# Kernel tuning notes

Hardware: AMD Instinct MI355X
Metric: run time of the kernel (lower is better)

## Reference

```python
import jax, jax.numpy as jnp
import numpy as np

N_NODES = 50000

def setup_inputs() -> dict:
    key = jax.random.key(0)
    ks = jax.random.split(key, 9)
    x = jax.random.normal(ks[0], (N_NODES, 100), dtype=jnp.float32)
    W0 = jax.random.normal(ks[1], (100, 64), dtype=jnp.float32) * (1.0 / np.sqrt(100))
    b0 = jnp.zeros((64,), dtype=jnp.float32)
    W1 = jax.random.normal(ks[2], (64, 64), dtype=jnp.float32) * (1.0 / np.sqrt(64))
    b1 = jnp.zeros((64,), dtype=jnp.float32)
    W2 = jax.random.normal(ks[3], (64, 47), dtype=jnp.float32) * (1.0 / np.sqrt(64))
    b2 = jnp.zeros((47,), dtype=jnp.float32)
    src = jax.random.randint(ks[4], (800000,), 0, N_NODES, dtype=jnp.int64)
    dst = jax.random.randint(ks[5], (800000,), 0, N_NODES, dtype=jnp.int64)
    return {"x": x, "W0": W0, "b0": b0, "W1": W1, "b1": b1,
            "W2": W2, "b2": b2, "src": src, "dst": dst}

def _degree_norms(src, dst, n_nodes):
    ones = jnp.ones(src.shape[0], dtype=jnp.float32)
    deg_out = jax.ops.segment_sum(ones, src, num_segments=n_nodes)
    deg_in = jax.ops.segment_sum(ones, dst, num_segments=n_nodes)
    # DGL GraphConv norm='both': clamp degree to >= 1 then D^{-1/2}
    norm_src = jax.lax.rsqrt(jnp.maximum(deg_out, 1.0))  # [N]
    norm_dst = jax.lax.rsqrt(jnp.maximum(deg_in, 1.0))   # [N]
    return norm_src, norm_dst

def _graph_conv(h, W, b, src, dst, norm_src, norm_dst, n_nodes):
    # h: [N, F_in] -> D_in^{-1/2} A D_out^{-1/2} h W + b
    m = h * norm_src[:, None]                              # [N, F_in]
    agg = jax.ops.segment_sum(m[src], dst, num_segments=n_nodes)  # SpMM gather/scatter
    agg = agg * norm_dst[:, None]
    return agg @ W + b

def reference(x, W0, b0, W1, b1, W2, b2, src, dst):
    n = x.shape[0]
    norm_src, norm_dst = _degree_norms(src, dst, n)
    # dropout is identity in eval mode (deterministic reference)
    h = jax.nn.relu(_graph_conv(x, W0, b0, src, dst, norm_src, norm_dst, n))
    h = jax.nn.relu(_graph_conv(h, W1, b1, src, dst, norm_src, norm_dst, n))
    out = _graph_conv(h, W2, b2, src, dst, norm_src, norm_dst, n)
    return out
```

## Files before the change

### kernel.cpp

```cpp
#include <hip/hip_runtime.h>
#include <hip/hip_fp16.h>
#include <stdint.h>


#define NNODES 50000
#define NBW    12500
#define HT     1024
#define EPT    7
#define EPB    (HT * EPT)

struct __align__(8) h4pack { __half2 a, b; };

__global__ __launch_bounds__(HT) void hist_kernel(
        const int* __restrict__ src, const int* __restrict__ dst,
        unsigned* __restrict__ cnt_dst, unsigned* __restrict__ cnt_src,
        unsigned char* __restrict__ rank, int E) {
    __shared__ unsigned h[NBW];
    const int b = blockIdx.x, base = b * EPB;
    int s[EPT], d[EPT]; bool val[EPT]; unsigned char rk[EPT];
    #pragma unroll
    for (int j = 0; j < EPT; ++j) {
        int e = base + j * HT + (int)threadIdx.x;
        val[j] = (e < E);
        s[j] = val[j] ? src[e] : 0;
        d[j] = val[j] ? dst[e] : 0;
        rk[j] = 0;
    }
    for (int w = threadIdx.x; w < NBW; w += HT) h[w] = 0u;
    __syncthreads();
    #pragma unroll
    for (int j = 0; j < EPT; ++j) if (val[j]) {
        unsigned sh = 8u * (d[j] & 3);
        unsigned old = atomicAdd(&h[d[j] >> 2], 1u << sh);
        rk[j] = (unsigned char)((old >> sh) & 0xffu);
    }
    __syncthreads();
    for (int w = threadIdx.x; w < NBW; w += HT) {
        cnt_dst[(size_t)b * NBW + w] = h[w];
        h[w] = 0u;
    }
    __syncthreads();
    #pragma unroll
    for (int j = 0; j < EPT; ++j) if (val[j])
        atomicAdd(&h[s[j] >> 2], 1u << (8u * (s[j] & 3)));
    #pragma unroll
    for (int j = 0; j < EPT; ++j) {
        int e = base + j * HT + (int)threadIdx.x;
        if (val[j]) rank[e] = rk[j];
    }
    __syncthreads();
    for (int w = threadIdx.x; w < NBW; w += HT)
        cnt_src[(size_t)b * NBW + w] = h[w];
}

__global__ __launch_bounds__(1024) void merge_scan_kernel(
        unsigned* __restrict__ cnt_dst, const unsigned* __restrict__ cnt_src,
        int* __restrict__ row_off, int* __restrict__ blocksum,
        float* __restrict__ ns, float* __restrict__ nd, int hb) {
    const int t = threadIdx.x;
    const int half = t & 511;
    const int w = blockIdx.x * 512 + half;
    const bool is_dst = (t < 512);
    unsigned deg[4] = {0, 0, 0, 0};
    if (w < NBW) {
        if (is_dst) {
            for (int b = 0; b < hb; ++b) {
                unsigned v = cnt_dst[(size_t)b * NBW + w];
                cnt_dst[(size_t)b * NBW + w] =
                    deg[0] | (deg[1] << 8) | (deg[2] << 16) | (deg[3] << 24);
                #pragma unroll
                for (int k = 0; k < 4; ++k) deg[k] += (v >> (8 * k)) & 0xffu;
            }
            #pragma unroll
            for (int k = 0; k < 4; ++k)
                nd[4 * w + k] = rsqrtf((float)(deg[k] < 1u ? 1u : deg[k]));
        } else {
            for (int b = 0; b < hb; ++b) {
                unsigned v = cnt_src[(size_t)b * NBW + w];
                #pragma unroll
                for (int k = 0; k < 4; ++k) deg[k] += (v >> (8 * k)) & 0xffu;
            }
            #pragma unroll
            for (int k = 0; k < 4; ++k)
                ns[4 * w + k] = rsqrtf((float)(deg[k] < 1u ? 1u : deg[k]));
        }
    }
    __shared__ int wsum[8];
    int sum = (is_dst && w < NBW) ? (int)(deg[0] + deg[1] + deg[2] + deg[3]) : 0;
    int lane = t & 63, wv = t >> 6;
    int incl = sum;
    #pragma unroll
    for (int off = 1; off < 64; off <<= 1) {
        int x = __shfl_up(incl, off, 64);
        if (lane >= off) incl += x;
    }
    if (is_dst && lane == 63) wsum[wv] = incl;
    __syncthreads();
    if (t < 8) {
        int v = wsum[t], ic = v;
        #pragma unroll
        for (int off = 1; off < 8; off <<= 1) {
            int x = __shfl_up(ic, off, 8);
            if ((t & 7) >= off) ic += x;
        }
        wsum[t] = ic;
    }
    __syncthreads();
    if (is_dst && w < NBW) {
        int base = (wv > 0 ? wsum[wv - 1] : 0) + incl - sum;
        row_off[4 * w + 0] = base;
        row_off[4 * w + 1] = base + (int)deg[0];
        row_off[4 * w + 2] = base + (int)(deg[0] + deg[1]);
        row_off[4 * w + 3] = base + (int)(deg[0] + deg[1] + deg[2]);
    }
    if (t == 0) blocksum[blockIdx.x] = wsum[7];
}

__global__ void scan2_kernel(const int* __restrict__ blocksum,
                             int* __restrict__ blockoff, int nb) {
    int i = threadIdx.x;
    int v = (i < nb) ? blocksum[i] : 0;
    int incl = v;
    #pragma unroll
    for (int off = 1; off < 64; off <<= 1) {
        int x = __shfl_up(incl, off, 64);
        if (i >= off) incl += x;
    }
    if (i < nb) blockoff[i] = incl - v;
}

__global__ __launch_bounds__(HT) void scatter_kernel(
        const int* __restrict__ src, const int* __restrict__ dst,
        const unsigned* __restrict__ cnt_dst, const int* __restrict__ row_off,
        const int* __restrict__ blockoff, const unsigned char* __restrict__ rank,
        unsigned short* __restrict__ src_sorted, int E) {
    const int b = blockIdx.x, base = b * EPB;
    #pragma unroll
    for (int j = 0; j < EPT; ++j) {
        int e = base + j * HT + (int)threadIdx.x;
        if (e >= E) continue;
        int d = dst[e];
        unsigned pk = cnt_dst[(size_t)b * NBW + (d >> 2)];
        unsigned pfx = (pk >> (8u * (d & 3))) & 0xffu;
        unsigned p = (unsigned)(row_off[d] + blockoff[d >> 11]) + pfx + (unsigned)rank[e];
        src_sorted[p] = (unsigned short)src[e];
    }
}

__global__ __launch_bounds__(256) void row_sort_kernel(
        const int* __restrict__ row_off, const int* __restrict__ blockoff,
        unsigned short* __restrict__ srcs, int n, int E) {
    int node = (blockIdx.x * 256 + threadIdx.x) >> 6;
    int lane = threadIdx.x & 63;
    if (node >= n) return;
    int beg = row_off[node] + blockoff[node >> 11];
    int end = (node + 1 < n) ? row_off[node + 1] + blockoff[(node + 1) >> 11] : E;
    int len = end - beg;
    if (len <= 1) return;
    unsigned v = (lane < len) ? (unsigned)srcs[beg + lane] : 0xffffffffu;
    #pragma unroll
    for (int k = 2; k <= 64; k <<= 1) {
        #pragma unroll
        for (int j = k >> 1; j >= 1; j >>= 1) {
            unsigned o = __shfl_xor(v, j, 64);
            bool down  = (lane & k) != 0;
            bool lower = (lane & j) == 0;
            unsigned mn = (v < o) ? v : o;
            unsigned mx = (v < o) ? o : v;
            v = (lower != down) ? mn : mx;
        }
    }
    if (lane < len) srcs[beg + lane] = (unsigned short)v;
}

template <int FIN, int FOUT>
__global__ __launch_bounds__(256) void rowscale_gemm_h(const float* __restrict__ H,
        const float* __restrict__ ns, const float* __restrict__ Wg,
        __half* __restrict__ T, int n) {
    constexpr int WS = (FOUT + 3) & ~3;
    constexpr int RP = FIN + 4;
    constexpr int Q  = FIN / 4;
    __shared__ __align__(16) float Wlds[FIN * WS];
    __shared__ __align__(16) float rows[64 * RP];

    for (int i = threadIdx.x; i < FIN * WS; i += 256) {
        int k = i / WS, j = i - k * WS;
        Wlds[i] = (j < FOUT) ? Wg[k * FOUT + j] : 0.0f;
    }
    int node0 = blockIdx.x * 64;
    for (int idx = threadIdx.x; idx < 64 * Q; idx += 256) {
        int nl = idx / Q, q = idx - nl * Q;
        int node = node0 + nl;
        float4 v = make_float4(0.f, 0.f, 0.f, 0.f);
        float s = 0.f;
        if (node < n) {
            v = *(const float4*)&H[(size_t)node * FIN + 4 * q];
            s = ns[node];
        }
        float4* d4 = (float4*)&rows[nl * RP + 4 * q];
        d4->x = v.x * s; d4->y = v.y * s; d4->z = v.z * s; d4->w = v.w * s;
    }
    __syncthreads();

    int w = threadIdx.x >> 6;
    int lane = threadIdx.x & 63;
    int g = lane >> 4, f = lane & 15;
    if (4 * f < WS) {
        float4 acc0 = make_float4(0.f,0.f,0.f,0.f), acc1 = acc0, acc2 = acc0, acc3 = acc0;
        const float* r0 = &rows[(w * 16 + 0 * 4 + g) * RP];
        const float* r1 = &rows[(w * 16 + 1 * 4 + g) * RP];
        const float* r2 = &rows[(w * 16 + 2 * 4 + g) * RP];
        const float* r3 = &rows[(w * 16 + 3 * 4 + g) * RP];
        for (int k = 0; k < FIN; ++k) {
            float4 wv = *(const float4*)&Wlds[k * WS + 4 * f];
            float h0 = r0[k], h1 = r1[k], h2 = r2[k], h3 = r3[k];
            acc0.x += h0 * wv.x; acc0.y += h0 * wv.y; acc0.z += h0 * wv.z; acc0.w += h0 * wv.w;
            acc1.x += h1 * wv.x; acc1.y += h1 * wv.y; acc1.z += h1 * wv.z; acc1.w += h1 * wv.w;
            acc2.x += h2 * wv.x; acc2.y += h2 * wv.y; acc2.z += h2 * wv.z; acc2.w += h2 * wv.w;
            acc3.x += h3 * wv.x; acc3.y += h3 * wv.y; acc3.z += h3 * wv.z; acc3.w += h3 * wv.w;
        }
        float4 accs[4] = {acc0, acc1, acc2, acc3};
        #pragma unroll
        for (int r = 0; r < 4; ++r) {
            int node = node0 + w * 16 + r * 4 + g;
            if (node < n) {
                h4pack pk;
                pk.a = __float22half2_rn(make_float2(accs[r].x, accs[r].y));
                pk.b = __float22half2_rn(make_float2(accs[r].z, accs[r].w));
                *(h4pack*)&T[(size_t)node * WS + 4 * f] = pk;
            }
        }
    }
}

__global__ __launch_bounds__(256) void agg_mid_kernel(const __half* __restrict__ T,
        const int* __restrict__ row_off, const int* __restrict__ blockoff,
        const unsigned short* __restrict__ srcs, const float* __restrict__ nd,
        const float* __restrict__ bias, float* __restrict__ H, int n, int E) {
    int node = (blockIdx.x * 256 + threadIdx.x) >> 6;
    int lane = threadIdx.x & 63;
    int g = lane >> 4, f = lane & 15;
    if (node >= n) return;
    int beg = row_off[node] + blockoff[node >> 11];
    int end = (node + 1 < n) ? row_off[node + 1] + blockoff[(node + 1) >> 11] : E;
    float4 acc = make_float4(0.f, 0.f, 0.f, 0.f);
    float4 acc2 = acc;
    int e = beg + g;
    for (; e + 4 < end; e += 8) {
        int s0 = srcs[e], s1 = srcs[e + 4];
        h4pack r0 = *(const h4pack*)&T[(size_t)s0 * 64 + 4 * f];
        h4pack r1 = *(const h4pack*)&T[(size_t)s1 * 64 + 4 * f];
        float2 a0 = __half22float2(r0.a), a1 = __half22float2(r0.b);
        float2 b0 = __half22float2(r1.a), b1 = __half22float2(r1.b);
        acc.x  += a0.x; acc.y  += a0.y; acc.z  += a1.x; acc.w  += a1.y;
        acc2.x += b0.x; acc2.y += b0.y; acc2.z += b1.x; acc2.w += b1.y;
    }
    if (e < end) {
        h4pack r0 = *(const h4pack*)&T[(size_t)srcs[e] * 64 + 4 * f];
        float2 a0 = __half22float2(r0.a), a1 = __half22float2(r0.b);
        acc.x += a0.x; acc.y += a0.y; acc.z += a1.x; acc.w += a1.y;
    }
    acc.x += acc2.x; acc.y += acc2.y; acc.z += acc2.z; acc.w += acc2.w;
    #pragma unroll
    for (int m = 16; m <= 32; m <<= 1) {
        acc.x += __shfl_xor(acc.x, m, 64);
        acc.y += __shfl_xor(acc.y, m, 64);
        acc.z += __shfl_xor(acc.z, m, 64);
        acc.w += __shfl_xor(acc.w, m, 64);
    }
    if (g == 0) {
        float sd = nd[node];
        float4 o;
        o.x = fmaxf(fmaf(acc.x, sd, bias[4 * f + 0]), 0.f);
        o.y = fmaxf(fmaf(acc.y, sd, bias[4 * f + 1]), 0.f);
        o.z = fmaxf(fmaf(acc.z, sd, bias[4 * f + 2]), 0.f);
        o.w = fmaxf(fmaf(acc.w, sd, bias[4 * f + 3]), 0.f);
        *(float4*)&H[(size_t)node * 64 + 4 * f] = o;
    }
}

__global__ __launch_bounds__(256) void agg_final_kernel(const __half* __restrict__ T,
        const int* __restrict__ row_off, const int* __restrict__ blockoff,
        const unsigned short* __restrict__ srcs, const float* __restrict__ nd,
        const float* __restrict__ bias, float* __restrict__ Out, int n, int E) {
    int node = (blockIdx.x * 256 + threadIdx.x) >> 6;
    int lane = threadIdx.x & 63;
    int g = lane >> 4, f = lane & 15;
    if (node >= n) return;
    int beg = row_off[node] + blockoff[node >> 11];
    int end = (node + 1 < n) ? row_off[node + 1] + blockoff[(node + 1) >> 11] : E;
    float4 acc = make_float4(0.f, 0.f, 0.f, 0.f);
    float4 acc2 = acc;
    if (f < 12) {
        int e = beg + g;
        for (; e + 4 < end; e += 8) {
            int s0 = srcs[e], s1 = srcs[e + 4];
            h4pack r0 = *(const h4pack*)&T[(size_t)s0 * 48 + 4 * f];
            h4pack r1 = *(const h4pack*)&T[(size_t)s1 * 48 + 4 * f];
            float2 a0 = __half22float2(r0.a), a1 = __half22float2(r0.b);
            float2 b0 = __half22float2(r1.a), b1 = __half22float2(r1.b);
            acc.x  += a0.x; acc.y  += a0.y; acc.z  += a1.x; acc.w  += a1.y;
            acc2.x += b0.x; acc2.y += b0.y; acc2.z += b1.x; acc2.w += b1.y;
        }
        if (e < end) {
            h4pack r0 = *(const h4pack*)&T[(size_t)srcs[e] * 48 + 4 * f];
            float2 a0 = __half22float2(r0.a), a1 = __half22float2(r0.b);
            acc.x += a0.x; acc.y += a0.y; acc.z += a1.x; acc.w += a1.y;
        }
    }
    acc.x += acc2.x; acc.y += acc2.y; acc.z += acc2.z; acc.w += acc2.w;
    #pragma unroll
    for (int m = 16; m <= 32; m <<= 1) {
        acc.x += __shfl_xor(acc.x, m, 64);
        acc.y += __shfl_xor(acc.y, m, 64);
        acc.z += __shfl_xor(acc.z, m, 64);
        acc.w += __shfl_xor(acc.w, m, 64);
    }
    if (g == 0 && f < 12) {
        float sd = nd[node];
        float a[4] = {acc.x, acc.y, acc.z, acc.w};
        #pragma unroll
        for (int j = 0; j < 4; ++j) {
            int c = 4 * f + j;
            if (c < 47)
                Out[(size_t)node * 47 + c] = fmaf(a[j], sd, bias[c]);
        }
    }
}

extern "C" void kernel_launch(void* const* d_in, const int* in_sizes, int n_in,
                              void* d_out, int out_size, void* d_ws, size_t ws_size,
                              hipStream_t stream) {
    const float* x  = (const float*)d_in[0];
    const float* W0 = (const float*)d_in[1];
    const float* b0 = (const float*)d_in[2];
    const float* W1 = (const float*)d_in[3];
    const float* b1 = (const float*)d_in[4];
    const float* W2 = (const float*)d_in[5];
    const float* b2 = (const float*)d_in[6];
    const int* src  = (const int*)d_in[7];
    const int* dst  = (const int*)d_in[8];
    float* out = (float*)d_out;

    const int N = NNODES;
    const int E = in_sizes[7];
    const int hb = (E + EPB - 1) / EPB;
    const int nchunk = (NBW + 511) / 512;

    unsigned* u = (unsigned*)d_ws;
    unsigned* cnt_dst = u;  u += (size_t)hb * NBW;
    unsigned* cnt_src = u;  u += (size_t)hb * NBW;
    int* p = (int*)u;
    int* row_off  = p;  p += N;
    int* blocksum = p;  p += 64;
    int* blockoff = p;  p += 64;
    unsigned char*  rank       = (unsigned char*)p;
    unsigned short* src_sorted = (unsigned short*)(rank + E);
    uintptr_t fp = ((uintptr_t)(src_sorted + E) + 15) & ~(uintptr_t)15;
    float* f = (float*)fp;
    float* norm_src = f;  f += N;
    float* norm_dst = f;  f += N;
    float* h_buf    = f;  f += (size_t)N * 64;
    __half* t01 = (__half*)f;
    __half* t2  = t01 + (size_t)N * 64;

    hist_kernel<<<hb, HT, 0, stream>>>(src, dst, cnt_dst, cnt_src, rank, E);
    merge_scan_kernel<<<nchunk, 1024, 0, stream>>>(cnt_dst, cnt_src, row_off,
                                                   blocksum, norm_src, norm_dst, hb);
    scan2_kernel<<<1, 64, 0, stream>>>(blocksum, blockoff, nchunk);
    scatter_kernel<<<hb, HT, 0, stream>>>(src, dst, cnt_dst, row_off, blockoff,
                                          rank, src_sorted, E);
    row_sort_kernel<<<(NNODES * 64 + 255) / 256, 256, 0, stream>>>(
        row_off, blockoff, src_sorted, N, E);

    const int gemm_grid = (N + 63) / 64;
    const int agg_grid  = (N * 64 + 255) / 256;

    rowscale_gemm_h<100, 64><<<gemm_grid, 256, 0, stream>>>(x, norm_src, W0, t01, N);
    agg_mid_kernel<<<agg_grid, 256, 0, stream>>>(t01, row_off, blockoff, src_sorted,
                                                 norm_dst, b0, h_buf, N, E);
    rowscale_gemm_h<64, 64><<<gemm_grid, 256, 0, stream>>>(h_buf, norm_src, W1, t01, N);
    agg_mid_kernel<<<agg_grid, 256, 0, stream>>>(t01, row_off, blockoff, src_sorted,
                                                 norm_dst, b1, h_buf, N, E);
    rowscale_gemm_h<64, 47><<<gemm_grid, 256, 0, stream>>>(h_buf, norm_src, W2, t2, N);
    agg_final_kernel<<<agg_grid, 256, 0, stream>>>(t2, row_off, blockoff, src_sorted,
                                                   norm_dst, b2, out, N, E);
}
```

Measured before the change: 218.0 us.

## Merge CSR scatter and first-layer GEMM into one heterogeneous launch

The scatter kernel and the first rowscale GEMM are independent, so they now run as one grid: the first hb blocks do the edge scatter (with 256 threads, each handling more edges) and the remaining blocks run the GEMM body. This removes one kernel launch and lets the memory-bound scatter overlap with the compute of the first GEMM. In exchange, scatter blocks now carry the GEMM's large LDS footprint, which can lower occupancy, and the scatter block size drops from 1024 to 256 threads.

After: 202.6 us. 7.1% less time.

```diff
diff --git a/kernel.cpp b/kernel.cpp
--- a/kernel.cpp
+++ b/kernel.cpp
@@ -129,54 +129,10 @@
     if (i < nb) blockoff[i] = incl - v;
 }
 
-__global__ __launch_bounds__(HT) void scatter_kernel(
-        const int* __restrict__ src, const int* __restrict__ dst,
-        const unsigned* __restrict__ cnt_dst, const int* __restrict__ row_off,
-        const int* __restrict__ blockoff, const unsigned char* __restrict__ rank,
-        unsigned short* __restrict__ src_sorted, int E) {
-    const int b = blockIdx.x, base = b * EPB;
-    #pragma unroll
-    for (int j = 0; j < EPT; ++j) {
-        int e = base + j * HT + (int)threadIdx.x;
-        if (e >= E) continue;
-        int d = dst[e];
-        unsigned pk = cnt_dst[(size_t)b * NBW + (d >> 2)];
-        unsigned pfx = (pk >> (8u * (d & 3))) & 0xffu;
-        unsigned p = (unsigned)(row_off[d] + blockoff[d >> 11]) + pfx + (unsigned)rank[e];
-        src_sorted[p] = (unsigned short)src[e];
-    }
-}
-
-__global__ __launch_bounds__(256) void row_sort_kernel(
-        const int* __restrict__ row_off, const int* __restrict__ blockoff,
-        unsigned short* __restrict__ srcs, int n, int E) {
-    int node = (blockIdx.x * 256 + threadIdx.x) >> 6;
-    int lane = threadIdx.x & 63;
-    if (node >= n) return;
-    int beg = row_off[node] + blockoff[node >> 11];
-    int end = (node + 1 < n) ? row_off[node + 1] + blockoff[(node + 1) >> 11] : E;
-    int len = end - beg;
-    if (len <= 1) return;
-    unsigned v = (lane < len) ? (unsigned)srcs[beg + lane] : 0xffffffffu;
-    #pragma unroll
-    for (int k = 2; k <= 64; k <<= 1) {
-        #pragma unroll
-        for (int j = k >> 1; j >= 1; j >>= 1) {
-            unsigned o = __shfl_xor(v, j, 64);
-            bool down  = (lane & k) != 0;
-            bool lower = (lane & j) == 0;
-            unsigned mn = (v < o) ? v : o;
-            unsigned mx = (v < o) ? o : v;
-            v = (lower != down) ? mn : mx;
-        }
-    }
-    if (lane < len) srcs[beg + lane] = (unsigned short)v;
-}
-
 template <int FIN, int FOUT>
-__global__ __launch_bounds__(256) void rowscale_gemm_h(const float* __restrict__ H,
+__device__ __forceinline__ void gemm_body(const float* __restrict__ H,
         const float* __restrict__ ns, const float* __restrict__ Wg,
-        __half* __restrict__ T, int n) {
+        __half* __restrict__ T, int n, int bblk) {
     constexpr int WS = (FOUT + 3) & ~3;
     constexpr int RP = FIN + 4;
     constexpr int Q  = FIN / 4;
@@ -187,7 +143,7 @@
         int k = i / WS, j = i - k * WS;
         Wlds[i] = (j < FOUT) ? Wg[k * FOUT + j] : 0.0f;
     }
-    int node0 = blockIdx.x * 64;
+    int node0 = bblk * 64;
     for (int idx = threadIdx.x; idx < 64 * Q; idx += 256) {
         int nl = idx / Q, q = idx - nl * Q;
         int node = node0 + nl;
@@ -231,6 +187,64 @@
             }
         }
     }
+}
+
+__global__ __launch_bounds__(256) void scatter_gemm_kernel(
+        const int* __restrict__ src, const int* __restrict__ dst,
+        const unsigned* __restrict__ cnt_dst, const int* __restrict__ row_off,
+        const int* __restrict__ blockoff, const unsigned char* __restrict__ rank,
+        unsigned short* __restrict__ src_sorted, int E, int sblocks,
+        const float* __restrict__ H, const float* __restrict__ ns,
+        const float* __restrict__ Wg, __half* __restrict__ T, int n) {
+    if ((int)blockIdx.x < sblocks) {
+        const int b = blockIdx.x, base = b * EPB;
+        const int t = threadIdx.x;
+        #pragma unroll
+        for (int j = 0; j < EPB / 256; ++j) {
+            int e = base + j * 256 + t;
+            if (e >= E) continue;
+            int d = dst[e];
+            unsigned pk = cnt_dst[(size_t)b * NBW + (d >> 2)];
+            unsigned pfx = (pk >> (8u * (d & 3))) & 0xffu;
+            unsigned p = (unsigned)(row_off[d] + blockoff[d >> 11]) + pfx + (unsigned)rank[e];
+            src_sorted[p] = (unsigned short)src[e];
+        }
+    } else {
+        gemm_body<100, 64>(H, ns, Wg, T, n, (int)blockIdx.x - sblocks);
+    }
+}
+
+__global__ __launch_bounds__(256) void row_sort_kernel(
+        const int* __restrict__ row_off, const int* __restrict__ blockoff,
+        unsigned short* __restrict__ srcs, int n, int E) {
+    int node = (blockIdx.x * 256 + threadIdx.x) >> 6;
+    int lane = threadIdx.x & 63;
+    if (node >= n) return;
+    int beg = row_off[node] + blockoff[node >> 11];
+    int end = (node + 1 < n) ? row_off[node + 1] + blockoff[(node + 1) >> 11] : E;
+    int len = end - beg;
+    if (len <= 1) return;
+    unsigned v = (lane < len) ? (unsigned)srcs[beg + lane] : 0xffffffffu;
+    #pragma unroll
+    for (int k = 2; k <= 64; k <<= 1) {
+        #pragma unroll
+        for (int j = k >> 1; j >= 1; j >>= 1) {
+            unsigned o = __shfl_xor(v, j, 64);
+            bool down  = (lane & k) != 0;
+            bool lower = (lane & j) == 0;
+            unsigned mn = (v < o) ? v : o;
+            unsigned mx = (v < o) ? o : v;
+            v = (lower != down) ? mn : mx;
+        }
+    }
+    if (lane < len) srcs[beg + lane] = (unsigned short)v;
+}
+
+template <int FIN, int FOUT>
+__global__ __launch_bounds__(256) void rowscale_gemm_h(const float* __restrict__ H,
+        const float* __restrict__ ns, const float* __restrict__ Wg,
+        __half* __restrict__ T, int n) {
+    gemm_body<FIN, FOUT>(H, ns, Wg, T, n, (int)blockIdx.x);
 }
 
 __global__ __launch_bounds__(256) void agg_mid_kernel(const __half* __restrict__ T,
@@ -364,19 +378,17 @@
     __half* t01 = (__half*)f;
     __half* t2  = t01 + (size_t)N * 64;
 
+    const int gemm_grid = (N + 63) / 64;
+    const int agg_grid  = (N * 64 + 255) / 256;
+
     hist_kernel<<<hb, HT, 0, stream>>>(src, dst, cnt_dst, cnt_src, rank, E);
     merge_scan_kernel<<<nchunk, 1024, 0, stream>>>(cnt_dst, cnt_src, row_off,
                                                    blocksum, norm_src, norm_dst, hb);
     scan2_kernel<<<1, 64, 0, stream>>>(blocksum, blockoff, nchunk);
-    scatter_kernel<<<hb, HT, 0, stream>>>(src, dst, cnt_dst, row_off, blockoff,
-                                          rank, src_sorted, E);
-    row_sort_kernel<<<(NNODES * 64 + 255) / 256, 256, 0, stream>>>(
-        row_off, blockoff, src_sorted, N, E);
-
-    const int gemm_grid = (N + 63) / 64;
-    const int agg_grid  = (N * 64 + 255) / 256;
-
-    rowscale_gemm_h<100, 64><<<gemm_grid, 256, 0, stream>>>(x, norm_src, W0, t01, N);
+    scatter_gemm_kernel<<<hb + gemm_grid, 256, 0, stream>>>(
+        src, dst, cnt_dst, row_off, blockoff, rank, src_sorted, E, hb,
+        x, norm_src, W0, t01, N);
+    row_sort_kernel<<<agg_grid, 256, 0, stream>>>(row_off, blockoff, src_sorted, N, E);
     agg_mid_kernel<<<agg_grid, 256, 0, stream>>>(t01, row_off, blockoff, src_sorted,
                                                  norm_dst, b0, h_buf, N, E);
     rowscale_gemm_h<64, 64><<<gemm_grid, 256, 0, stream>>>(h_buf, norm_src, W1, t01, N);
```
